# Optimization experiments

Hardware: AMD Instinct MI355X
Metric: run time of the kernel (lower is better)

## Reference

```python
import jax, jax.numpy as jnp
import numpy as np

N = 100000      # nodes
E = 1600000     # directed edges
F_IN = 128      # num_node_features
H = 256         # hidden_dim
OUT = 128       # output_dim
G = 2048        # number of graphs in batch
EPS = 1e-5      # BatchNorm eps


def setup_inputs() -> dict:
    key = jax.random.key(0)
    ks = jax.random.split(key, 8)
    x = jax.random.normal(ks[0], (N, F_IN), jnp.float32)
    row = jax.random.randint(ks[1], (E,), 0, N, dtype=jnp.int32)
    col = jax.random.randint(ks[2], (E,), 0, N, dtype=jnp.int32)
    batch = jnp.sort(jax.random.randint(ks[3], (N,), 0, G, dtype=jnp.int32))

    def lin(k, fi, fo):
        return (jax.random.normal(k, (fi, fo), jnp.float32) / np.sqrt(fi)).astype(jnp.float32)

    return {
        "x": x, "row": row, "col": col, "batch": batch,
        "W1": lin(ks[4], F_IN, H), "b1": jnp.zeros((H,), jnp.float32),
        "g1": jnp.ones((H,), jnp.float32), "be1": jnp.zeros((H,), jnp.float32),
        "W2": lin(ks[5], H, H), "b2": jnp.zeros((H,), jnp.float32),
        "g2": jnp.ones((H,), jnp.float32), "be2": jnp.zeros((H,), jnp.float32),
        "W3": lin(ks[6], H, OUT), "b3": jnp.zeros((OUT,), jnp.float32),
        "g3": jnp.ones((OUT,), jnp.float32), "be3": jnp.zeros((OUT,), jnp.float32),
    }


def gcn_conv(x, W, b, row, col):
    # PyG GCNConv: add self-loops, symmetric deg normalization, then scatter-add.
    h = x @ W                                              # [N, F_out]
    deg = jnp.ones((N,), x.dtype).at[col].add(jnp.ones((E,), x.dtype))  # +1 for self-loop
    dinv = jax.lax.rsqrt(deg)                              # deg >= 1, safe
    norm = dinv[row] * dinv[col]                           # [E]
    agg = jnp.zeros_like(h).at[col].add(h[row] * norm[:, None])
    agg = agg + h * (dinv * dinv)[:, None]                 # self-loop messages
    return agg + b


def batchnorm(x, g, b):
    # training-mode batch statistics (running stats at init are 0/1 anyway)
    m = x.mean(axis=0)
    v = x.var(axis=0)
    return g * (x - m) * jax.lax.rsqrt(v + EPS) + b


def reference(x, row, col, batch, W1, b1, g1, be1, W2, b2, g2, be2, W3, b3, g3, be3):
    h = jax.nn.relu(batchnorm(gcn_conv(x, W1, b1, row, col), g1, be1))
    h = jax.nn.relu(batchnorm(gcn_conv(h, W2, b2, row, col), g2, be2))
    h = batchnorm(gcn_conv(h, W3, b3, row, col), g3, be3)
    # global_mean_pool over graphs
    sums = jax.ops.segment_sum(h, batch, num_segments=G)   # [G, OUT]
    cnt = jax.ops.segment_sum(jnp.ones((N,), h.dtype), batch, num_segments=G)
    return sums / jnp.maximum(cnt, 1.0)[:, None]
```

## Files before the change

kernel.cpp:

```cpp
#include <hip/hip_runtime.h>

#define NN 100000
#define EE 1600000
#define GG 2048
#define EPSB 1e-5f
#define MP 100096
#define MBLK (MP / 128)
#define NB 782
#define CAP 2560
#define CAPP 3584

typedef unsigned short u16;
typedef __attribute__((ext_vector_type(8))) short short8;
typedef __attribute__((ext_vector_type(4))) float f32x4;

struct alignas(4)  u16x2 { u16 v[2]; };
struct alignas(8)  u16x4 { u16 v[4]; };
struct alignas(16) u16x8 { u16 v[8]; };

__device__ __forceinline__ float b2f(u16 u) { return __uint_as_float(((unsigned)u) << 16); }
__device__ __forceinline__ u16 f2b(float f) {
    unsigned u = __float_as_uint(f);
    return (u16)((u + 0x7FFF + ((u >> 16) & 1)) >> 16);
}
__device__ __forceinline__ void gload16(const void* g, void* l) {
    __builtin_amdgcn_global_load_lds((const __attribute__((address_space(1))) void*)g,
                                     (__attribute__((address_space(3))) void*)l, 16, 0, 0);
}


#define ZB0 (NB * 16)
#define ZB1 (ZB0 + 1280)
#define ZB2 (ZB1 + 1)
#define ZB3 (ZB2 + (MP - NN) * 64)
#define ZB4 (ZB3 + (MP - NN) * 128)

__global__ void init_kernel(unsigned* __restrict__ bcur, unsigned* __restrict__ statsAll,
                            unsigned* __restrict__ dinvNN, unsigned* __restrict__ padA128,
                            unsigned* __restrict__ padA256) {
    int i = blockIdx.x * 256 + threadIdx.x;
    if (i < ZB0) bcur[i] = 0u;
    else if (i < ZB1) statsAll[i - ZB0] = 0u;
    else if (i < ZB2) dinvNN[0] = 0u;
    else if (i < ZB3) padA128[i - ZB2] = 0u;
    else if (i < ZB4) padA256[i - ZB3] = 0u;
}


__global__ void bucketA_kernel(const int* __restrict__ row, const int* __restrict__ col,
                               int* __restrict__ bcur, unsigned* __restrict__ bkt) {
    int e = blockIdx.x * 256 + threadIdx.x;
    if (e < EE) {
        int c = col[e], r = row[e];
        int b = c >> 7;
        int p = atomicAdd(&bcur[b * 16], 1);
        if (p < CAP) bkt[(size_t)b * CAP + p] = ((unsigned)r << 7) | (unsigned)(c & 127);
    }
}

__global__ void bucketBC_kernel(const unsigned* __restrict__ bkt, const int* __restrict__ bcur,
                                int* __restrict__ begs, int* __restrict__ ends,
                                float* __restrict__ dinv, int* __restrict__ srcs) {
    int b = blockIdx.x, t = threadIdx.x;
    __shared__ int lcnt[128];
    __shared__ int sp[128];
    __shared__ int cur[128];
    if (t < 128) lcnt[t] = 0;
    __syncthreads();
    int tot = bcur[b * 16];
    if (tot > CAP) tot = CAP;
    const unsigned* B = bkt + (size_t)b * CAP;
    for (int i = t; i < tot; i += 256) atomicAdd(&lcnt[(int)(B[i] & 127u)], 1);
    __syncthreads();
    int n0 = b << 7;
    int pc = 0;
    if (t < 128) {
        int rc = lcnt[t];
        if (n0 + t < NN) dinv[n0 + t] = rsqrtf((float)(rc + 1));
        pc = (rc + 7) & ~7;
        sp[t] = pc;
    }
    __syncthreads();
    for (int o = 1; o < 128; o <<= 1) {
        int u = (t >= o && t < 128) ? sp[t - o] : 0;
        __syncthreads();
        if (t < 128) sp[t] += u;
        __syncthreads();
    }
    int base = b * CAPP;
    if (t < 128) {
        int st = base + sp[t] - pc;
        cur[t] = st;
        if (n0 + t < NN) { begs[n0 + t] = st; ends[n0 + t] = st + pc; }
    }
    __syncthreads();
    for (int i = t; i < tot; i += 256) {
        unsigned v = B[i];
        int p = atomicAdd(&cur[(int)(v & 127u)], 1);
        srcs[p] = (int)(v >> 7);
    }
    __syncthreads();
    if (t < 128 && n0 + t < NN) {
        int st = cur[t];
        int en = base + sp[t];
        for (int i = st; i < en; ++i) srcs[i] = NN;
    }
}


__global__ void xwcast_kernel(const float* __restrict__ x, u16* __restrict__ xb,
                              const float* __restrict__ W1, const float* __restrict__ W2,
                              const float* __restrict__ W3, u16* __restrict__ Wt1,
                              u16* __restrict__ Wt2, u16* __restrict__ Wt3) {
    int idx = blockIdx.x * 256 + threadIdx.x;
    if (idx < NN * 32) {
        float4 v = ((const float4*)x)[idx];
        u16x4 o = {{f2b(v.x), f2b(v.y), f2b(v.z), f2b(v.w)}};
        ((u16x4*)xb)[idx] = o;
        return;
    }
    int j = idx - NN * 32;
    if (j < 32768) {
        int n = j >> 7, k = j & 127;
        Wt1[j] = f2b(W1[k * 256 + n]);
    } else if (j < 98304) {
        int jj = j - 32768;
        int n = jj >> 8, k = jj & 255;
        Wt2[jj] = f2b(W2[k * 256 + n]);
    } else if (j < 131072) {
        int jj = j - 98304;
        int n = jj >> 8, k = jj & 255;
        Wt3[jj] = f2b(W3[k * 128 + n]);
    }
}


template <int F, bool TR>
__global__ void agg_kernel(const u16* __restrict__ X, u16* __restrict__ out,
                           const int* __restrict__ begs, const int* __restrict__ ends,
                           const int* __restrict__ srcs, const float* __restrict__ dinv,
                           const float* __restrict__ sc, const float* __restrict__ shf) {
    constexpr int VE = F / 64;
    int node = blockIdx.x * 4 + (threadIdx.x >> 6);
    if (node >= NN) return;
    int l = threadIdx.x & 63;
    int f0 = l * VE;
    float s_[VE], t_[VE];
    if (TR) {
#pragma unroll
        for (int j = 0; j < VE; ++j) { s_[j] = sc[f0 + j]; t_[j] = shf[f0 + j]; }
    }
    float acc[VE] = {};
    int beg = begs[node], end = ends[node];

    auto fetch = [&](int s, u16* u) {
        if (VE == 4) *(u16x4*)u = *(const u16x4*)(X + (size_t)s * F + f0);
        else         *(u16x2*)u = *(const u16x2*)(X + (size_t)s * F + f0);
    };
    auto accum = [&](const u16* u, float w) {
#pragma unroll
        for (int j = 0; j < VE; ++j) {
            float v = b2f(u[j]);
            if (TR) v = fmaxf(fmaf(s_[j], v, t_[j]), 0.f);
            acc[j] = fmaf(w, v, acc[j]);
        }
    };

    for (int e0 = beg; e0 < end; e0 += 64) {
        int take = end - e0;
        if (take > 64) take = 64;
        int sv = (l < take) ? srcs[e0 + l] : NN;
        float wv = dinv[sv];
        for (int j = 0; j < take; j += 8) {
            int s[8];
            float w[8];
            u16 u[8][VE];
#pragma unroll
            for (int q = 0; q < 8; ++q) {
                s[q] = __shfl(sv, j + q);
                w[q] = __shfl(wv, j + q);
            }
#pragma unroll
            for (int q = 0; q < 8; ++q) fetch(s[q], u[q]);
#pragma unroll
            for (int q = 0; q < 8; ++q) accum(u[q], w[q]);
        }
    }
    float di = dinv[node];
    u16 us[VE];
    fetch(node, us);
    accum(us, di);
    if (VE == 4) {
        u16x4 o = {{f2b(di * acc[0]), f2b(di * acc[1]), f2b(di * acc[2]), f2b(di * acc[3])}};
        *(u16x4*)(out + (size_t)node * F + f0) = o;
    } else {
        u16x2 o = {{f2b(di * acc[0]), f2b(di * acc[1])}};
        *(u16x2*)(out + (size_t)node * F + f0) = o;
    }
}


template <bool STATS, bool FUSEA>
__global__ __launch_bounds__(256) void gemm_kernel(const u16* __restrict__ A,
                                                   const u16* __restrict__ Wt,
                                                   u16* __restrict__ C,
                                                   int Kdim, int Nout,
                                                   float* __restrict__ gstats,
                                                   const float* __restrict__ sc,
                                                   const float* __restrict__ shf) {
    __shared__ u16 As[128 * 64];
    __shared__ u16 Bs[128 * 64];
    __shared__ float sbuf[2][128];
    const int tid = threadIdx.x;
    const int w = tid >> 6, l = tid & 63;
    const int row0 = blockIdx.x * 128;
    const int col0 = blockIdx.y * 128;
    const int srow = w * 32 + (l >> 3);
    const int skel = (l & 7) * 8;
    const u16* Asrc = A + (size_t)(row0 + srow) * Kdim + skel;
    const u16* Bsrc = Wt + (size_t)(col0 + srow) * Kdim + skel;
    u16* AsBase = &As[w * 2048];
    u16* BsBase = &Bs[w * 2048];
    const int wr = (w >> 1) * 64, wc = (w & 1) * 64;
    f32x4 acc[4][4] = {};
    if (STATS && tid < 128) { sbuf[0][tid] = 0.f; sbuf[1][tid] = 0.f; }

    for (int k0 = 0; k0 < Kdim; k0 += 64) {
        if (FUSEA) {
            float4 sa0 = *(const float4*)&sc[k0 + skel];
            float4 sa1 = *(const float4*)&sc[k0 + skel + 4];
            float4 ta0 = *(const float4*)&shf[k0 + skel];
            float4 ta1 = *(const float4*)&shf[k0 + skel + 4];
            float sA[8] = {sa0.x, sa0.y, sa0.z, sa0.w, sa1.x, sa1.y, sa1.z, sa1.w};
            float tA[8] = {ta0.x, ta0.y, ta0.z, ta0.w, ta1.x, ta1.y, ta1.z, ta1.w};
#pragma unroll
            for (int j = 0; j < 4; ++j) {
                u16x8 av = *(const u16x8*)(Asrc + (size_t)(j * 8) * Kdim + k0);
                u16x8 o;
#pragma unroll
                for (int i = 0; i < 8; ++i)
                    o.v[i] = f2b(fmaxf(fmaf(sA[i], b2f(av.v[i]), tA[i]), 0.f));
                *(u16x8*)&As[(w * 32 + j * 8 + (l >> 3)) * 64 + skel] = o;
            }
        } else {
#pragma unroll
            for (int j = 0; j < 4; ++j)
                gload16(Asrc + (size_t)(j * 8) * Kdim + k0, AsBase + j * 512);
        }
#pragma unroll
        for (int j = 0; j < 4; ++j)
            gload16(Bsrc + (size_t)(j * 8) * Kdim + k0, BsBase + j * 512);
        __syncthreads();
#pragma unroll
        for (int ks = 0; ks < 2; ++ks) {
            short8 a[4], b[4];
#pragma unroll
            for (int mi = 0; mi < 4; ++mi)
                a[mi] = *(const short8*)&As[(wr + mi * 16 + (l & 15)) * 64 + ks * 32 + (l >> 4) * 8];
#pragma unroll
            for (int ni = 0; ni < 4; ++ni)
                b[ni] = *(const short8*)&Bs[(wc + ni * 16 + (l & 15)) * 64 + ks * 32 + (l >> 4) * 8];
#pragma unroll
            for (int mi = 0; mi < 4; ++mi)
#pragma unroll
                for (int ni = 0; ni < 4; ++ni)
                    acc[mi][ni] = __builtin_amdgcn_mfma_f32_16x16x32_bf16(a[mi], b[ni], acc[mi][ni], 0, 0, 0);
        }
        __syncthreads();
    }
    const int cr = (l >> 4) * 4, cc = l & 15;
#pragma unroll
    for (int mi = 0; mi < 4; ++mi) {
#pragma unroll
        for (int j = 0; j < 4; ++j) {
            int r = row0 + wr + mi * 16 + cr + j;
#pragma unroll
            for (int ni = 0; ni < 4; ++ni)
                C[(size_t)r * Nout + col0 + wc + ni * 16 + cc] = f2b(acc[mi][ni][j]);
        }
    }
    if (STATS) {
#pragma unroll
        for (int ni = 0; ni < 4; ++ni) {
            float s = 0.f, q = 0.f;
#pragma unroll
            for (int mi = 0; mi < 4; ++mi)
#pragma unroll
                for (int jj = 0; jj < 4; ++jj) {
                    float v = acc[mi][ni][jj];
                    s += v;
                    q += v * v;
                }
            s += __shfl_xor(s, 16); s += __shfl_xor(s, 32);
            q += __shfl_xor(q, 16); q += __shfl_xor(q, 32);
            if (l < 16) {
                atomicAdd(&sbuf[0][wc + ni * 16 + l], s);
                atomicAdd(&sbuf[1][wc + ni * 16 + l], q);
            }
        }
        __syncthreads();
        if (tid < 128) {
            atomicAdd(&gstats[col0 + tid], sbuf[0][tid]);
            atomicAdd(&gstats[Nout + col0 + tid], sbuf[1][tid]);
        }
    }
}


__global__ void finalize_kernel(const float* __restrict__ sums, int F,
                                const float* __restrict__ g, const float* __restrict__ be,
                                float* __restrict__ sc, float* __restrict__ shf) {
    int f = threadIdx.x;
    if (f < F) {
        float m = sums[f] * (1.f / NN);
        float v = sums[F + f] * (1.f / NN) - m * m;
        float s = g[f] * rsqrtf(v + EPSB);
        sc[f] = s;
        shf[f] = be[f] - m * s;
    }
}


__global__ void poolstats_kernel(const u16* __restrict__ Z, const int* __restrict__ batch,
                                 float* __restrict__ gsum, int* __restrict__ gcnt,
                                 float* __restrict__ sums) {
    int gph = blockIdx.x;
    int f = threadIdx.x;
    __shared__ int sb, se;
    if (f == 0) {
        int lo = 0, hi = NN;
        while (lo < hi) { int mid = (lo + hi) >> 1; if (batch[mid] < gph) lo = mid + 1; else hi = mid; }
        sb = lo;
        hi = NN;
        while (lo < hi) { int mid = (lo + hi) >> 1; if (batch[mid] < gph + 1) lo = mid + 1; else hi = mid; }
        se = lo;
    }
    __syncthreads();
    int beg = sb, end = se;
    float acc = 0.f, qq = 0.f;
    for (int r = beg; r < end; ++r) {
        float v = b2f(Z[(size_t)r * 128 + f]);
        acc += v;
        qq += v * v;
    }
    gsum[(size_t)gph * 128 + f] = acc;
    if (f == 0) gcnt[gph] = end - beg;
    atomicAdd(&sums[f], acc);
    atomicAdd(&sums[128 + f], qq);
}

__global__ void poolout_kernel(const float* __restrict__ gsum, const int* __restrict__ gcnt,
                               const float* __restrict__ sc, const float* __restrict__ shf,
                               float* __restrict__ out) {
    int i = blockIdx.x * 256 + threadIdx.x;
    if (i < GG * 128) {
        int g = i >> 7, f = i & 127;
        int c = gcnt[g];
        out[i] = (c > 0) ? fmaf(sc[f], gsum[i] / (float)c, shf[f]) : 0.f;
    }
}


extern "C" void kernel_launch(void* const* d_in, const int* in_sizes, int n_in,
                              void* d_out, int out_size, void* d_ws, size_t ws_size,
                              hipStream_t stream) {
    const float* x     = (const float*)d_in[0];
    const int*   row   = (const int*)d_in[1];
    const int*   col   = (const int*)d_in[2];
    const int*   batch = (const int*)d_in[3];
    const float* W1 = (const float*)d_in[4];
    const float* g1 = (const float*)d_in[6];
    const float* be1 = (const float*)d_in[7];
    const float* W2 = (const float*)d_in[8];
    const float* g2 = (const float*)d_in[10];
    const float* be2 = (const float*)d_in[11];
    const float* W3 = (const float*)d_in[12];
    const float* g3 = (const float*)d_in[14];
    const float* be3 = (const float*)d_in[15];
    float* out = (float*)d_out;

    char* ws = (char*)d_ws;
    size_t off = 0;
    auto alloc = [&](size_t bytes) { size_t o = off; off += (bytes + 255) & ~255ULL; return o; };
    u16*   bufA   = (u16*)  (ws + alloc((size_t)MP * 256 * 2));
    u16*   bufB   = (u16*)  (ws + alloc((size_t)MP * 256 * 2));
    u16*   xb     = (u16*)  (ws + alloc((size_t)MP * 128 * 2));
    u16*   Wt1    = (u16*)  (ws + alloc(128 * 256 * 2));
    u16*   Wt2    = (u16*)  (ws + alloc(256 * 256 * 2));
    u16*   Wt3    = (u16*)  (ws + alloc(256 * 128 * 2));
    int*   begs   = (int*)  (ws + alloc((size_t)(NN + 16) * 4));
    int*   ends   = (int*)  (ws + alloc((size_t)(NN + 16) * 4));
    float* dinv   = (float*)(ws + alloc((size_t)(NN + 16) * 4));
    int*   srcs   = (int*)  (ws + alloc((size_t)NB * CAPP * 4));
    unsigned* bkt = (unsigned*)(ws + alloc((size_t)NB * CAP * 4));
    int*   bcur   = (int*)  (ws + alloc((size_t)NB * 16 * 4));
    float* statsAll = (float*)(ws + alloc(1280 * 4));
    float* scbuf  = (float*)(ws + alloc(6 * 256 * 4));
    float* gsum   = (float*)(ws + alloc((size_t)GG * 128 * 4));
    int*   gcnt   = (int*)  (ws + alloc((size_t)GG * 4));

    init_kernel<<<(ZB4 + 255) / 256, 256, 0, stream>>>(
        (unsigned*)bcur, (unsigned*)statsAll, (unsigned*)&dinv[NN],
        (unsigned*)(bufA + (size_t)NN * 128), (unsigned*)(bufA + (size_t)NN * 256));

    bucketA_kernel<<<(EE + 255) / 256, 256, 0, stream>>>(row, col, bcur, bkt);
    bucketBC_kernel<<<NB, 256, 0, stream>>>(bkt, bcur, begs, ends, dinv, srcs);

    xwcast_kernel<<<(NN * 32 + 131072 + 255) / 256, 256, 0, stream>>>(
        x, xb, W1, W2, W3, Wt1, Wt2, Wt3);

    const int aggBlocks = (NN + 3) / 4;

    agg_kernel<128, false><<<aggBlocks, 256, 0, stream>>>(xb, bufA, begs, ends, srcs, dinv, nullptr, nullptr);
    gemm_kernel<true, false><<<dim3(MBLK, 2), 256, 0, stream>>>(bufA, Wt1, bufB, 128, 256, statsAll, nullptr, nullptr);
    finalize_kernel<<<1, 256, 0, stream>>>(statsAll, 256, g1, be1, scbuf + 0, scbuf + 256);

    agg_kernel<256, true><<<aggBlocks, 256, 0, stream>>>(bufB, bufA, begs, ends, srcs, dinv, scbuf + 0, scbuf + 256);
    gemm_kernel<true, false><<<dim3(MBLK, 2), 256, 0, stream>>>(bufA, Wt2, bufB, 256, 256, statsAll + 512, nullptr, nullptr);
    finalize_kernel<<<1, 256, 0, stream>>>(statsAll + 512, 256, g2, be2, scbuf + 512, scbuf + 768);

    gemm_kernel<false, true><<<dim3(MBLK, 1), 256, 0, stream>>>(bufB, Wt3, bufA, 256, 128, nullptr, scbuf + 512, scbuf + 768);
    agg_kernel<128, false><<<aggBlocks, 256, 0, stream>>>(bufA, xb, begs, ends, srcs, dinv, nullptr, nullptr);
    poolstats_kernel<<<GG, 128, 0, stream>>>(xb, batch, gsum, gcnt, statsAll + 1024);
    finalize_kernel<<<1, 256, 0, stream>>>(statsAll + 1024, 128, g3, be3, scbuf + 1024, scbuf + 1280);
    poolout_kernel<<<(GG * 128 + 255) / 256, 256, 0, stream>>>(gsum, gcnt, scbuf + 1024, scbuf + 1280, out);
}
```

Measured before the change: 564.1 us.

## Sort CSR sources in LDS, narrow agg groups for F=128, fold final BN into pool

The CSR build now assembles each bucket in shared memory, insertion-sorts each node's source list for locality, and writes it out contiguously. The aggregation kernel is templated on group width, so the 128-feature passes use 32-lane groups (8 nodes per block, 4 features per lane) to cut wasted lanes and shuffle overhead. The last finalize kernel is dropped by computing the BatchNorm scale and shift inline in poolout. The risk is the serial per-thread insertion sort and the larger LDS footprint slowing down the CSR build.

```diff
diff --git a/kernel.cpp b/kernel.cpp
--- a/kernel.cpp
+++ b/kernel.cpp
@@ -65,6 +65,7 @@
     __shared__ int lcnt[128];
     __shared__ int sp[128];
     __shared__ int cur[128];
+    __shared__ int sarr[CAPP];
     if (t < 128) lcnt[t] = 0;
     __syncthreads();
     int tot = bcur[b * 16];
@@ -73,9 +74,9 @@
     for (int i = t; i < tot; i += 256) atomicAdd(&lcnt[(int)(B[i] & 127u)], 1);
     __syncthreads();
     int n0 = b << 7;
-    int pc = 0;
+    int pc = 0, rc = 0;
     if (t < 128) {
-        int rc = lcnt[t];
+        rc = lcnt[t];
         if (n0 + t < NN) dinv[n0 + t] = rsqrtf((float)(rc + 1));
         pc = (rc + 7) & ~7;
         sp[t] = pc;
@@ -87,24 +88,32 @@
         if (t < 128) sp[t] += u;
         __syncthreads();
     }
-    int base = b * CAPP;
+    int stl = 0;
     if (t < 128) {
-        int st = base + sp[t] - pc;
-        cur[t] = st;
-        if (n0 + t < NN) { begs[n0 + t] = st; ends[n0 + t] = st + pc; }
+        stl = sp[t] - pc;
+        cur[t] = stl;
     }
     __syncthreads();
     for (int i = t; i < tot; i += 256) {
         unsigned v = B[i];
         int p = atomicAdd(&cur[(int)(v & 127u)], 1);
-        srcs[p] = (int)(v >> 7);
-    }
-    __syncthreads();
-    if (t < 128 && n0 + t < NN) {
-        int st = cur[t];
-        int en = base + sp[t];
-        for (int i = st; i < en; ++i) srcs[i] = NN;
-    }
+        sarr[p] = (int)(v >> 7);
+    }
+    __syncthreads();
+    if (t < 128) {
+        for (int i = stl + rc; i < stl + pc; ++i) sarr[i] = NN;
+        for (int i = stl + 1; i < stl + rc; ++i) {
+            int key = sarr[i];
+            int j = i - 1;
+            while (j >= stl && sarr[j] > key) { sarr[j + 1] = sarr[j]; --j; }
+            sarr[j + 1] = key;
+        }
+    }
+    __syncthreads();
+    int base = b * CAPP;
+    int total = sp[127];
+    for (int i = t; i < total; i += 256) srcs[base + i] = sarr[i];
+    if (t < 128 && n0 + t < NN) { begs[n0 + t] = base + stl; ends[n0 + t] = base + stl + pc; }
 }
 
 
@@ -135,15 +144,16 @@
 }
 
 
-template <int F, bool TR>
+template <int F, int GROUP, bool TR>
 __global__ void agg_kernel(const u16* __restrict__ X, u16* __restrict__ out,
                            const int* __restrict__ begs, const int* __restrict__ ends,
                            const int* __restrict__ srcs, const float* __restrict__ dinv,
                            const float* __restrict__ sc, const float* __restrict__ shf) {
-    constexpr int VE = F / 64;
-    int node = blockIdx.x * 4 + (threadIdx.x >> 6);
+    constexpr int VE = F / GROUP;
+    constexpr int NPB = 256 / GROUP;
+    int node = blockIdx.x * NPB + threadIdx.x / GROUP;
     if (node >= NN) return;
-    int l = threadIdx.x & 63;
+    int l = threadIdx.x & (GROUP - 1);
     int f0 = l * VE;
     float s_[VE], t_[VE];
     if (TR) {
@@ -166,9 +176,9 @@
         }
     };
 
-    for (int e0 = beg; e0 < end; e0 += 64) {
+    for (int e0 = beg; e0 < end; e0 += GROUP) {
         int take = end - e0;
-        if (take > 64) take = 64;
+        if (take > GROUP) take = GROUP;
         int sv = (l < take) ? srcs[e0 + l] : NN;
         float wv = dinv[sv];
         for (int j = 0; j < take; j += 8) {
@@ -177,8 +187,8 @@
             u16 u[8][VE];
 #pragma unroll
             for (int q = 0; q < 8; ++q) {
-                s[q] = __shfl(sv, j + q);
-                w[q] = __shfl(wv, j + q);
+                s[q] = __shfl(sv, j + q, GROUP);
+                w[q] = __shfl(wv, j + q, GROUP);
             }
 #pragma unroll
             for (int q = 0; q < 8; ++q) fetch(s[q], u[q]);
@@ -350,13 +360,18 @@
 }
 
 __global__ void poolout_kernel(const float* __restrict__ gsum, const int* __restrict__ gcnt,
-                               const float* __restrict__ sc, const float* __restrict__ shf,
+                               const float* __restrict__ sums,
+                               const float* __restrict__ g, const float* __restrict__ be,
                                float* __restrict__ out) {
     int i = blockIdx.x * 256 + threadIdx.x;
     if (i < GG * 128) {
-        int g = i >> 7, f = i & 127;
-        int c = gcnt[g];
-        out[i] = (c > 0) ? fmaf(sc[f], gsum[i] / (float)c, shf[f]) : 0.f;
+        int gr = i >> 7, f = i & 127;
+        float m = sums[f] * (1.f / NN);
+        float v = sums[128 + f] * (1.f / NN) - m * m;
+        float scv = g[f] * rsqrtf(v + EPSB);
+        float shv = be[f] - m * scv;
+        int c = gcnt[gr];
+        out[i] = (c > 0) ? fmaf(scv, gsum[i] / (float)c, shv) : 0.f;
     }
 }
 
@@ -409,19 +424,16 @@
     xwcast_kernel<<<(NN * 32 + 131072 + 255) / 256, 256, 0, stream>>>(
         x, xb, W1, W2, W3, Wt1, Wt2, Wt3);
 
-    const int aggBlocks = (NN + 3) / 4;
-
-    agg_kernel<128, false><<<aggBlocks, 256, 0, stream>>>(xb, bufA, begs, ends, srcs, dinv, nullptr, nullptr);
+    agg_kernel<128, 32, false><<<NN / 8, 256, 0, stream>>>(xb, bufA, begs, ends, srcs, dinv, nullptr, nullptr);
     gemm_kernel<true, false><<<dim3(MBLK, 2), 256, 0, stream>>>(bufA, Wt1, bufB, 128, 256, statsAll, nullptr, nullptr);
     finalize_kernel<<<1, 256, 0, stream>>>(statsAll, 256, g1, be1, scbuf + 0, scbuf + 256);
 
-    agg_kernel<256, true><<<aggBlocks, 256, 0, stream>>>(bufB, bufA, begs, ends, srcs, dinv, scbuf + 0, scbuf + 256);
+    agg_kernel<256, 64, true><<<NN / 4, 256, 0, stream>>>(bufB, bufA, begs, ends, srcs, dinv, scbuf + 0, scbuf + 256);
     gemm_kernel<true, false><<<dim3(MBLK, 2), 256, 0, stream>>>(bufA, Wt2, bufB, 256, 256, statsAll + 512, nullptr, nullptr);
     finalize_kernel<<<1, 256, 0, stream>>>(statsAll + 512, 256, g2, be2, scbuf + 512, scbuf + 768);
 
     gemm_kernel<false, true><<<dim3(MBLK, 1), 256, 0, stream>>>(bufB, Wt3, bufA, 256, 128, nullptr, scbuf + 512, scbuf + 768);
-    agg_kernel<128, false><<<aggBlocks, 256, 0, stream>>>(bufA, xb, begs, ends, srcs, dinv, nullptr, nullptr);
+    agg_kernel<128, 32, false><<<NN / 8, 256, 0, stream>>>(bufA, xb, begs, ends, srcs, dinv, nullptr, nullptr);
     poolstats_kernel<<<GG, 128, 0, stream>>>(xb, batch, gsum, gcnt, statsAll + 1024);
-    finalize_kernel<<<1, 256, 0, stream>>>(statsAll + 1024, 128, g3, be3, scbuf + 1024, scbuf + 1280);
-    poolout_kernel<<<(GG * 128 + 255) / 256, 256, 0, stream>>>(gsum, gcnt, scbuf + 1024, scbuf + 1280, out);
-}
+    poolout_kernel<<<(GG * 128 + 255) / 256, 256, 0, stream>>>(gsum, gcnt, statsAll + 1024, g3, be3, out);
+}
```

Result: slower. 594.3 us (+5.4%).
